# Kernel optimization log

Measured on AMD Instinct MI355X. Metric: run time of the kernel, lower is better.

## Reference

```python
import jax, jax.numpy as jnp
import numpy as np

V_SIZES = [2562, 10242, 40962]
E_SIZES = [7680, 30720, 122880]
NG = 8000


def _chamfer(a, b):
    # a: [Na,3], b: [Nb,3] -> squared NN distances (dist_a:[Na], dist_b:[Nb])
    # ||a-b||^2 = ||a||^2 + ||b||^2 - 2 a.b  (GEMM form, same math as pairwise diff)
    an = jnp.sum(a * a, axis=-1)
    bn = jnp.sum(b * b, axis=-1)
    d = an[:, None] + bn[None, :] - 2.0 * (a @ b.T)  # [Na,Nb]
    d = jnp.maximum(d, 0.0)
    return d.min(axis=1), d.min(axis=0)


def _edge_regularization(pred, edges):
    # nn.MSELoss(reduction='none') over endpoint pairs, mean, scaled by coord dim
    diff = pred[edges[:, 0]] - pred[edges[:, 1]]  # [E,3]
    return jnp.mean(diff * diff) * pred.shape[-1]


def _laplace_coord(x, lap_idx):
    # x: [N,3]; lap_idx: [N,10] -> cols 0..7 neighbor idx (-1 pad), col 9 count
    nbr = lap_idx[:, :8]
    valid = nbr >= 0
    idx = jnp.where(valid, nbr, 0)
    v = x[idx]                                  # [N,8,3]
    v = jnp.where(valid[..., None], v, 0.0)
    cnt = lap_idx[:, -1].astype(x.dtype)
    return x - v.sum(axis=1) / cnt[:, None]


def _laplace_regularization(feats, pts, lap_idx):
    lap1 = _laplace_coord(feats, lap_idx)
    lap2 = _laplace_coord(pts, lap_idx)
    d = lap1 - lap2
    return jnp.mean(d * d) * lap1.shape[-1]


def _p2m_loss(pred_pts, pred_feats, gt, edges, lap_idx):
    lap_const = [0.2, 1.0, 1.0]
    chamfer_loss = 0.0
    edge_loss = 0.0
    lap_loss = 0.0
    for i in range(3):
        d1, d2 = _chamfer(gt, pred_pts[i])
        chamfer_loss = chamfer_loss + jnp.mean(d1) + jnp.mean(d2)
        edge_loss = edge_loss + _edge_regularization(pred_pts[i], edges[i])
        lap_loss = lap_loss + lap_const[i] * _laplace_regularization(pred_feats[i], pred_pts[i], lap_idx[i])
    loss = 100.0 * chamfer_loss + 0.1 * edge_loss + 0.3 * lap_loss
    return loss, chamfer_loss, edge_loss, lap_loss


def _make_lap_idx(key, V):
    k1, k2 = jax.random.split(key)
    nbr = jax.random.randint(k1, (V, 8), 0, V)
    mask = jax.random.uniform(k2, (V, 8)) < 0.8
    mask = mask.at[:, 0].set(True)  # at least one valid neighbor
    nbr = jnp.where(mask, nbr, -1)
    cnt = mask.sum(axis=1)
    dummy = jnp.zeros((V, 1), jnp.int32)
    return jnp.concatenate([nbr, dummy, cnt[:, None]], axis=1).astype(jnp.int32)


def setup_inputs() -> dict:
    key = jax.random.key(0)
    ks = jax.random.split(key, 16)
    inp = {}
    for i, V in enumerate(V_SIZES):
        inp[f"pred_pts_{i+1}"] = jax.random.normal(ks[i], (V, 3), dtype=jnp.float32)
        inp[f"pred_feats_{i+1}"] = jax.random.normal(ks[3 + i], (V, 3), dtype=jnp.float32)
        inp[f"edges_{i+1}"] = jax.random.randint(ks[6 + i], (E_SIZES[i], 2), 0, V).astype(jnp.int32)
        inp[f"lap_idx_{i+1}"] = _make_lap_idx(ks[9 + i], V)
    inp["gt_pts"] = jax.random.normal(ks[12], (1, NG, 3), dtype=jnp.float32)
    return inp


def reference(pred_pts_1, pred_pts_2, pred_pts_3,
              pred_feats_1, pred_feats_2, pred_feats_3,
              gt_pts,
              edges_1, edges_2, edges_3,
              lap_idx_1, lap_idx_2, lap_idx_3):
    gt = gt_pts.reshape(-1, 3)
    return _p2m_loss(
        [pred_pts_1, pred_pts_2, pred_pts_3],
        [pred_feats_1, pred_feats_2, pred_feats_3],
        gt,
        [edges_1, edges_2, edges_3],
        [lap_idx_1, lap_idx_2, lap_idx_3],
    )
```

## Files before the change

kernel.cpp:

```cpp
#include <hip/hip_runtime.h>

#define NG 8000
#define V1 2562
#define V2 10242
#define V3 40962
#define E1 7680
#define E2 30720
#define E3 122880
#define NPRED (V1 + V2 + V3)
#define NPK   (NG + NPRED)
#define ND1   (3 * NG)
#define NMIN  (ND1 + NPRED)
#define CHUNK 512
#define AAW   128
#define ABLK  512

typedef __attribute__((ext_vector_type(8))) short bf16x8;
typedef __attribute__((ext_vector_type(4))) float f32x4;

struct PassTab { int NA[6], NB[6], Aoff[6], Boff[6], ooff[6], xb[6], base[7]; };

__device__ __forceinline__ float min3f(float a, float b, float c) {
    float r;
    asm("v_min3_f32 %0, %1, %2, %3" : "=v"(r) : "v"(a), "v"(b), "v"(c));
    return r;
}

__device__ __forceinline__ unsigned short f2bf(float f) {
    unsigned int u = __float_as_uint(f);
    return (unsigned short)((u + 0x7fffu + ((u >> 16) & 1u)) >> 16);
}
__device__ __forceinline__ float bf2f(unsigned short b) {
    return __uint_as_float(((unsigned int)b) << 16);
}
__device__ __forceinline__ unsigned int pk(unsigned short lo, unsigned short hi) {
    return (unsigned int)lo | ((unsigned int)hi << 16);
}

__device__ __forceinline__ double block_reduce_add(double v, double* sm) {
    int lane = threadIdx.x & 63;
    int wid  = threadIdx.x >> 6;
    for (int off = 32; off > 0; off >>= 1) v += __shfl_down(v, off, 64);
    if (lane == 0) sm[wid] = v;
    __syncthreads();
    double r = 0.0;
    if (wid == 0) {
        int nw = blockDim.x >> 6;
        r = (lane < nw) ? sm[lane] : 0.0;
        for (int off = 32; off > 0; off >>= 1) r += __shfl_down(r, off, 64);
    }
    return r;
}

__global__ void k_prep(const float* __restrict__ gt,
                       const float* __restrict__ q1, const float* __restrict__ q2,
                       const float* __restrict__ q3,
                       uint4* __restrict__ Arec, uint4* __restrict__ Brec,
                       float* __restrict__ an, unsigned int* __restrict__ mins,
                       double* __restrict__ acc) {
    int stride = gridDim.x * blockDim.x;
    for (int i = blockIdx.x * blockDim.x + threadIdx.x; i < NMIN; i += stride) {
        if (i < 8) acc[i] = 0.0;
        mins[i] = 0x7f800000u;
        if (i < NPK) {
            const float* src; int k;
            if (i < NG) { src = gt; k = i; }
            else {
                int t = i - NG;
                if (t < V1)            { src = q1; k = t; }
                else if (t < V1 + V2)  { src = q2; k = t - V1; }
                else                   { src = q3; k = t - V1 - V2; }
            }
            float x = src[3 * k], y = src[3 * k + 1], z = src[3 * k + 2];
            unsigned short hx = f2bf(x), hy = f2bf(y), hz = f2bf(z);
            float hxf = bf2f(hx), hyf = bf2f(hy), hzf = bf2f(hz);
            unsigned short lx = f2bf(x - hxf), ly = f2bf(y - hyf), lz = f2bf(z - hzf);
            float bn = fmaf(x, x, fmaf(y, y, z * z));
            unsigned short bnh = f2bf(bn);
            unsigned short bnl = f2bf(bn - bf2f(bnh));
            unsigned short nhx = f2bf(-2.f * hxf), nhy = f2bf(-2.f * hyf), nhz = f2bf(-2.f * hzf);
            unsigned short nlx = f2bf(-2.f * bf2f(lx)), nly = f2bf(-2.f * bf2f(ly)), nlz = f2bf(-2.f * bf2f(lz));
            size_t p = (size_t)i;
            Arec[p * 4 + 0] = make_uint4(pk(nhx, nhy), pk(nhz, nhx), pk(nhy, nhz), pk(0x3F80, 0x3F80));
            Arec[p * 4 + 1] = make_uint4(pk(nlx, nly), pk(nlz, 0), 0u, 0u);
            Arec[p * 4 + 2] = make_uint4(0u, 0u, 0u, 0u);
            Arec[p * 4 + 3] = make_uint4(0u, 0u, 0u, 0u);
            Brec[p * 2 + 0] = make_uint4(pk(hx, hy), pk(hz, lx), pk(ly, lz), pk(bnh, bnl));
            Brec[p * 2 + 1] = make_uint4(pk(hx, hy), pk(hz, 0), 0u, 0u);
            an[i] = bn;
        }
    }
}

__launch_bounds__(256)
__global__ void k_pair_mfma(const uint4* __restrict__ Arec,
                            const uint4* __restrict__ Brec,
                            const float* __restrict__ an,
                            unsigned int* __restrict__ mins, PassTab T) {
    __shared__ uint4 sb[2 * CHUNK];
    int bid = blockIdx.x, tid = threadIdx.x;

    int p = 0;
    while (p < 5 && bid >= T.base[p + 1]) ++p;
    int rel  = bid - T.base[p];
    int xb   = T.xb[p];
    int xblk = rel % xb, yblk = rel / xb;
    int NA = T.NA[p], NB = T.NB[p];
    int Aoff = T.Aoff[p], Boff = T.Boff[p], ooff = T.ooff[p];

    int j0  = yblk * CHUNK;
    int cnt = min(NB - j0, CHUNK);

    for (int i = tid; i < 2 * CHUNK; i += 256) {
        int pt = i >> 1, gg = i & 1;
        uint4 v;
        if (pt < cnt) v = Brec[(size_t)(Boff + j0 + pt) * 2 + gg];
        else          v = gg ? make_uint4(0u, 0u, 0u, 0u)
                             : make_uint4(0u, 0u, 0u, 0x00007F80u);
        sb[i] = v;
    }
    __syncthreads();

    int l = tid & 63, w = tid >> 6;
    int g = l >> 4, c = l & 15;
    int Abase = xblk * ABLK + w * AAW;

    union U { uint4 u; bf16x8 b; };

    bf16x8 af[8];
    float  m[8];
#pragma unroll
    for (int tt = 0; tt < 8; ++tt) {
        int apt = Abase + tt * 16 + c;
        int ap  = min(apt, NA - 1);
        U u; u.u = Arec[(size_t)(Aoff + ap) * 4 + g];
        af[tt] = u.b;
        m[tt]  = __builtin_inff();
    }

    unsigned int msk = (g < 2) ? 0xFFFFFFFFu : 0u;
    const uint4* bbase = sb + (c * 2 + (g & 1));
    f32x4 zero = {0.f, 0.f, 0.f, 0.f};

    for (int jb = 0; jb < cnt; jb += 16) {
        uint4 r = bbase[jb * 2];
        r.x &= msk; r.y &= msk; r.z &= msk; r.w &= msk;
        U u; u.u = r;
        bf16x8 bfr = u.b;
#pragma unroll
        for (int tt = 0; tt < 8; ++tt) {
            f32x4 a = __builtin_amdgcn_mfma_f32_16x16x32_bf16(bfr, af[tt], zero, 0, 0, 0);
            float t0 = min3f(a[0], a[1], a[2]);
            m[tt] = min3f(m[tt], t0, a[3]);
        }
    }

#pragma unroll
    for (int tt = 0; tt < 8; ++tt) {
        float mm = m[tt];
        mm = fminf(mm, __shfl_xor(mm, 16, 64));
        mm = fminf(mm, __shfl_xor(mm, 32, 64));
        int apt = Abase + tt * 16 + c;
        if (g == 0 && apt < NA) {
            float d = fmaxf(an[Aoff + apt] + mm, 0.f);
            atomicMin(mins + ooff + apt, __float_as_uint(d));
        }
    }
}

#define R0 NMIN
#define R1 (E1 + E2 + E3)
#define R2 NPRED
__global__ void k_post(const unsigned int* __restrict__ mins,
                       const float* __restrict__ p1, const float* __restrict__ p2,
                       const float* __restrict__ p3,
                       const int* __restrict__ e1, const int* __restrict__ e2,
                       const int* __restrict__ e3,
                       const float* __restrict__ f1, const float* __restrict__ f2,
                       const float* __restrict__ f3,
                       const int* __restrict__ l1, const int* __restrict__ l2,
                       const int* __restrict__ l3,
                       double* __restrict__ acc) {
    __shared__ double sm[8];
    double s0 = 0.0, s1 = 0.0, s2 = 0.0;
    int stride = gridDim.x * blockDim.x;
    int gid = blockIdx.x * blockDim.x + threadIdx.x;
    for (int i = gid; i < R0 + R1 + R2; i += stride) {
        if (i < R0) {
            double w;
            if (i < ND1) w = 1.0 / NG;
            else {
                int t = i - ND1;
                w = (t < V1) ? (1.0 / V1) : ((t < V1 + V2) ? (1.0 / V2) : (1.0 / V3));
            }
            s0 += (double)__uint_as_float(mins[i]) * w;
        } else if (i < R0 + R1) {
            int q = i - R0;
            const float* p; const int* e; int k; double w;
            if (q < E1)            { p = p1; e = e1; k = q;            w = 1.0 / E1; }
            else if (q < E1 + E2)  { p = p2; e = e2; k = q - E1;       w = 1.0 / E2; }
            else                   { p = p3; e = e3; k = q - E1 - E2;  w = 1.0 / E3; }
            int u = e[2 * k], v = e[2 * k + 1];
            float dx = p[3 * u]     - p[3 * v];
            float dy = p[3 * u + 1] - p[3 * v + 1];
            float dz = p[3 * u + 2] - p[3 * v + 2];
            s1 += w * (double)(dx * dx + dy * dy + dz * dz);
        } else {
            int q = i - R0 - R1;
            const float* f; const float* p; const int* l; int k; double w;
            if (q < V1)            { f = f1; p = p1; l = l1; k = q;            w = 0.2 / V1; }
            else if (q < V1 + V2)  { f = f2; p = p2; l = l2; k = q - V1;       w = 1.0 / V2; }
            else                   { f = f3; p = p3; l = l3; k = q - V1 - V2;  w = 1.0 / V3; }
            const int* row = l + 10 * k;
            float sfx = 0.f, sfy = 0.f, sfz = 0.f, spx = 0.f, spy = 0.f, spz = 0.f;
#pragma unroll
            for (int r = 0; r < 8; ++r) {
                int n = row[r];
                if (n >= 0) {
                    sfx += f[3 * n]; sfy += f[3 * n + 1]; sfz += f[3 * n + 2];
                    spx += p[3 * n]; spy += p[3 * n + 1]; spz += p[3 * n + 2];
                }
            }
            float inv = 1.0f / (float)row[9];
            float dx = (f[3 * k]     - p[3 * k])     - (sfx - spx) * inv;
            float dy = (f[3 * k + 1] - p[3 * k + 1]) - (sfy - spy) * inv;
            float dz = (f[3 * k + 2] - p[3 * k + 2]) - (sfz - spz) * inv;
            s2 += w * (double)(dx * dx + dy * dy + dz * dz);
        }
    }
    double r0 = block_reduce_add(s0, sm); __syncthreads();
    double r1 = block_reduce_add(s1, sm); __syncthreads();
    double r2 = block_reduce_add(s2, sm);
    if (threadIdx.x == 0) {
        atomicAdd(acc + 0, r0);
        atomicAdd(acc + 1, r1);
        atomicAdd(acc + 2, r2);
    }
}

__global__ void k_final(const double* __restrict__ acc, float* __restrict__ out) {
    if (threadIdx.x == 0 && blockIdx.x == 0) {
        double ch = acc[0], ed = acc[1], lp = acc[2];
        out[0] = (float)(100.0 * ch + 0.1 * ed + 0.3 * lp);
        out[1] = (float)ch;
        out[2] = (float)ed;
        out[3] = (float)lp;
    }
}

static void build_tab(PassTab& T) {
    const int NAs[6]  = { NG, NG, NG, V1, V2, V3 };
    const int NBs[6]  = { V1, V2, V3, NG, NG, NG };
    const int AoP[6]  = { 0, 0, 0, NG, NG + V1, NG + V1 + V2 };
    const int BoP[6]  = { NG, NG + V1, NG + V1 + V2, 0, 0, 0 };
    const int ooP[6]  = { 0, NG, 2 * NG, ND1, ND1 + V1, ND1 + V1 + V2 };
    int base = 0;
    for (int p = 0; p < 6; ++p) {
        int xb = (NAs[p] + ABLK - 1) / ABLK;
        int ny = (NBs[p] + CHUNK - 1) / CHUNK;
        T.NA[p] = NAs[p]; T.NB[p] = NBs[p];
        T.Aoff[p] = AoP[p]; T.Boff[p] = BoP[p]; T.ooff[p] = ooP[p];
        T.xb[p] = xb; T.base[p] = base;
        base += xb * ny;
    }
    T.base[6] = base;
}

extern "C" void kernel_launch(void* const* d_in, const int* in_sizes, int n_in,
                              void* d_out, int out_size, void* d_ws, size_t ws_size,
                              hipStream_t stream) {
    const float *pp[3], *pf[3], *gt;
    const int *ed[3], *li[3];
    if (in_sizes[1] == 3 * V1) {
        pp[0] = (const float*)d_in[0];  pf[0] = (const float*)d_in[1];
        ed[0] = (const int*)d_in[2];    li[0] = (const int*)d_in[3];
        pp[1] = (const float*)d_in[4];  pf[1] = (const float*)d_in[5];
        ed[1] = (const int*)d_in[6];    li[1] = (const int*)d_in[7];
        pp[2] = (const float*)d_in[8];  pf[2] = (const float*)d_in[9];
        ed[2] = (const int*)d_in[10];   li[2] = (const int*)d_in[11];
        gt = (const float*)d_in[12];
    } else {
        pp[0] = (const float*)d_in[0];  pp[1] = (const float*)d_in[1];  pp[2] = (const float*)d_in[2];
        pf[0] = (const float*)d_in[3];  pf[1] = (const float*)d_in[4];  pf[2] = (const float*)d_in[5];
        gt    = (const float*)d_in[6];
        ed[0] = (const int*)d_in[7];    ed[1] = (const int*)d_in[8];    ed[2] = (const int*)d_in[9];
        li[0] = (const int*)d_in[10];   li[1] = (const int*)d_in[11];   li[2] = (const int*)d_in[12];
    }

    PassTab T;
    build_tab(T);

    char* ws = (char*)d_ws;
    double*       acc  = (double*)ws;
    unsigned int* mins = (unsigned int*)(ws + 1024);
    float*        an   = (float*)(ws + 400 * 1024);
    uint4*        Arec = (uint4*)(ws + 1024 * 1024);
    uint4*        Brec = (uint4*)(ws + 6 * 1024 * 1024);

    k_prep<<<256, 256, 0, stream>>>(gt, pp[0], pp[1], pp[2], Arec, Brec, an, mins, acc);
    k_pair_mfma<<<T.base[6], 256, 0, stream>>>(Arec, Brec, an, mins, T);
    k_post<<<256, 256, 0, stream>>>(mins, pp[0], pp[1], pp[2],
                                    ed[0], ed[1], ed[2],
                                    pf[0], pf[1], pf[2],
                                    li[0], li[1], li[2], acc);
    k_final<<<1, 64, 0, stream>>>(acc, (float*)d_out);
}
```

Before: 162.1 us.

## Switch pairwise chamfer MFMA from 16x16x32 to 32x32x16 bf16 tiles

```diff
diff --git a/kernel.cpp b/kernel.cpp
--- a/kernel.cpp
+++ b/kernel.cpp
@@ -15,16 +15,10 @@
 #define AAW   128
 #define ABLK  512
 
-typedef __attribute__((ext_vector_type(8))) short bf16x8;
-typedef __attribute__((ext_vector_type(4))) float f32x4;
+typedef __attribute__((ext_vector_type(8)))  short bf16x8;
+typedef __attribute__((ext_vector_type(16))) float f32x16;
 
 struct PassTab { int NA[6], NB[6], Aoff[6], Boff[6], ooff[6], xb[6], base[7]; };
-
-__device__ __forceinline__ float min3f(float a, float b, float c) {
-    float r;
-    asm("v_min3_f32 %0, %1, %2, %3" : "=v"(r) : "v"(a), "v"(b), "v"(c));
-    return r;
-}
 
 __device__ __forceinline__ unsigned short f2bf(float f) {
     unsigned int u = __float_as_uint(f);
@@ -81,10 +75,8 @@
             unsigned short nhx = f2bf(-2.f * hxf), nhy = f2bf(-2.f * hyf), nhz = f2bf(-2.f * hzf);
             unsigned short nlx = f2bf(-2.f * bf2f(lx)), nly = f2bf(-2.f * bf2f(ly)), nlz = f2bf(-2.f * bf2f(lz));
             size_t p = (size_t)i;
-            Arec[p * 4 + 0] = make_uint4(pk(nhx, nhy), pk(nhz, nhx), pk(nhy, nhz), pk(0x3F80, 0x3F80));
-            Arec[p * 4 + 1] = make_uint4(pk(nlx, nly), pk(nlz, 0), 0u, 0u);
-            Arec[p * 4 + 2] = make_uint4(0u, 0u, 0u, 0u);
-            Arec[p * 4 + 3] = make_uint4(0u, 0u, 0u, 0u);
+            Arec[p * 2 + 0] = make_uint4(pk(nhx, nhy), pk(nhz, nhx), pk(nhy, nhz), pk(0x3F80, 0x3F80));
+            Arec[p * 2 + 1] = make_uint4(pk(nlx, nly), pk(nlz, 0), 0u, 0u);
             Brec[p * 2 + 0] = make_uint4(pk(hx, hy), pk(hz, lx), pk(ly, lz), pk(bnh, bnl));
             Brec[p * 2 + 1] = make_uint4(pk(hx, hy), pk(hz, 0), 0u, 0u);
             an[i] = bn;
@@ -122,46 +114,48 @@
     __syncthreads();
 
     int l = tid & 63, w = tid >> 6;
-    int g = l >> 4, c = l & 15;
+    int half = l >> 5, c = l & 31;
     int Abase = xblk * ABLK + w * AAW;
 
     union U { uint4 u; bf16x8 b; };
 
-    bf16x8 af[8];
-    float  m[8];
+    bf16x8 af[4];
+    float  m[4];
 #pragma unroll
-    for (int tt = 0; tt < 8; ++tt) {
-        int apt = Abase + tt * 16 + c;
+    for (int tt = 0; tt < 4; ++tt) {
+        int apt = Abase + tt * 32 + c;
         int ap  = min(apt, NA - 1);
-        U u; u.u = Arec[(size_t)(Aoff + ap) * 4 + g];
+        U u; u.u = Arec[(size_t)(Aoff + ap) * 2 + half];
         af[tt] = u.b;
         m[tt]  = __builtin_inff();
     }
 
-    unsigned int msk = (g < 2) ? 0xFFFFFFFFu : 0u;
-    const uint4* bbase = sb + (c * 2 + (g & 1));
-    f32x4 zero = {0.f, 0.f, 0.f, 0.f};
-
-    for (int jb = 0; jb < cnt; jb += 16) {
-        uint4 r = bbase[jb * 2];
-        r.x &= msk; r.y &= msk; r.z &= msk; r.w &= msk;
-        U u; u.u = r;
+    f32x16 zero = {0.f};
+
+    for (int jb = 0; jb < cnt; jb += 32) {
+        U u; u.u = sb[(jb + c) * 2 + half];
         bf16x8 bfr = u.b;
 #pragma unroll
-        for (int tt = 0; tt < 8; ++tt) {
-            f32x4 a = __builtin_amdgcn_mfma_f32_16x16x32_bf16(bfr, af[tt], zero, 0, 0, 0);
-            float t0 = min3f(a[0], a[1], a[2]);
-            m[tt] = min3f(m[tt], t0, a[3]);
+        for (int tt = 0; tt < 4; ++tt) {
+            f32x16 d = __builtin_amdgcn_mfma_f32_32x32x16_bf16(bfr, af[tt], zero, 0, 0, 0);
+            float mm = m[tt];
+            mm = fminf(fminf(mm, d[0]),  d[1]);
+            mm = fminf(fminf(mm, d[2]),  d[3]);
+            mm = fminf(fminf(mm, d[4]),  d[5]);
+            mm = fminf(fminf(mm, d[6]),  d[7]);
+            mm = fminf(fminf(mm, d[8]),  d[9]);
+            mm = fminf(fminf(mm, d[10]), d[11]);
+            mm = fminf(fminf(mm, d[12]), d[13]);
+            mm = fminf(fminf(mm, d[14]), d[15]);
+            m[tt] = mm;
         }
     }
 
 #pragma unroll
-    for (int tt = 0; tt < 8; ++tt) {
-        float mm = m[tt];
-        mm = fminf(mm, __shfl_xor(mm, 16, 64));
-        mm = fminf(mm, __shfl_xor(mm, 32, 64));
-        int apt = Abase + tt * 16 + c;
-        if (g == 0 && apt < NA) {
+    for (int tt = 0; tt < 4; ++tt) {
+        float mm = fminf(m[tt], __shfl_xor(m[tt], 32, 64));
+        int apt = Abase + tt * 32 + c;
+        if (half == 0 && apt < NA) {
             float d = fmaxf(an[Aoff + apt] + mm, 0.f);
             atomicMin(mins + ooff + apt, __float_as_uint(d));
         }
@@ -295,7 +289,7 @@
     unsigned int* mins = (unsigned int*)(ws + 1024);
     float*        an   = (float*)(ws + 400 * 1024);
     uint4*        Arec = (uint4*)(ws + 1024 * 1024);
-    uint4*        Brec = (uint4*)(ws + 6 * 1024 * 1024);
+    uint4*        Brec = (uint4*)(ws + 4 * 1024 * 1024);
 
     k_prep<<<256, 256, 0, stream>>>(gt, pp[0], pp[1], pp[2], Arec, Brec, an, mins, acc);
     k_pair_mfma<<<T.base[6], 256, 0, stream>>>(Arec, Brec, an, mins, T);
```

New measurement: 143.5 us. 1.13x faster.
